# Performance work log

Hardware: AMD Instinct MI355X
Metric: run time of the kernel (lower is better)

## Reference

```python
import jax, jax.numpy as jnp
import numpy as np

N, D, K = 32768, 256, 4096
COMMITMENT_COST = 0.25
EPS_NORM = 1e-12  # matches torch F.normalize eps


def _l2_normalize(x):
    n = jnp.linalg.norm(x, axis=1, keepdims=True)
    return x / jnp.maximum(n, EPS_NORM)


def setup_inputs() -> dict:
    key = jax.random.key(0)
    k1, k2 = jax.random.split(key)
    inputs = jax.random.normal(k1, (N, D), dtype=jnp.float32)
    # xavier_uniform-like scale for the codebook
    bound = float(np.sqrt(6.0 / (K + D)))
    embeddings = jax.random.uniform(k2, (K, D), dtype=jnp.float32, minval=-bound, maxval=bound)
    return {"inputs": inputs, "embeddings": embeddings}


def reference(inputs, embeddings):
    flat = inputs.reshape(-1, D)
    x = _l2_normalize(flat)              # [N, D]
    e = _l2_normalize(embeddings)        # [K, D]
    # squared euclidean distance on normalized vectors
    distances = (jnp.sum(x * x, axis=1, keepdims=True)
                 + jnp.sum(e * e, axis=1)
                 - 2.0 * jnp.matmul(x, e.T))          # [N, K]
    encoding_indices = jnp.argmin(distances, axis=1)  # [N]
    quantized = embeddings[encoding_indices]          # gather, [N, D]
    # commitment loss (EMA variant: only commitment term is trained)
    e_latent_loss = jnp.mean((jax.lax.stop_gradient(quantized) - flat) ** 2)
    loss = COMMITMENT_COST * e_latent_loss
    # straight-through estimator
    quantized_st = flat + jax.lax.stop_gradient(quantized - flat)
    quantized_st = quantized_st.reshape(inputs.shape)
    return quantized_st, loss, encoding_indices
```

## Files before the change

### kernel.cpp

```cpp
#include <hip/hip_runtime.h>
#include <math.h>
#include <stdint.h>
#include <limits.h>

#define NPTS 32768
#define DIM  256
#define KCB  4096
#define NQ   (NPTS*DIM)

#define EPSN    1e-12f
#define MARGIN1 6.0e-4f
#define F16MIN  6.103515625e-05f
#define CAPB    4096
#define KINIT   0x7F800000FFFFFFFFull

typedef __attribute__((ext_vector_type(8))) _Float16 f16x8;
typedef __attribute__((ext_vector_type(4))) _Float16 f16x4;
typedef __attribute__((ext_vector_type(4))) float    f32x4;

#define WS_EH0   0u
#define WS_TRI   2097152u
#define WS_EMBT  0u
#define WS_SUME  4194304u
#define WS_EINV  4210688u
#define WS_XINV  4227072u
#define WS_IDX   4358144u
#define WS_RCA   4489216u
#define WS_RLA   4489232u
#define WS_RCB   4751376u
#define WS_RLB   4751392u
#define WS_BEST  4882464u
#define WS_LOSSP 4915232u

__device__ inline unsigned fbits(float f){ union{float f;unsigned u;}v; v.f=f; return v.u; }
__device__ inline float bitsf(unsigned u){ union{float f;unsigned u;}v; v.u=u; return v.f; }
__device__ inline uint64_t dbits(double d){ union{double d;uint64_t u;}v; v.d=d; return v.u; }
__device__ inline _Float16 g16(float v){
    return (fabsf(v) < F16MIN) ? (_Float16)0.0f : (_Float16)v;
}
__device__ inline void gload16(const void* src, void* lds){
    __builtin_amdgcn_global_load_lds((const __attribute__((address_space(1))) void*)src,
                                     (__attribute__((address_space(3))) void*)lds, 16, 0, 0);
}

__global__ void k_init(int* rca, int* rcb) {
    if (threadIdx.x == 0) { *rca = 0; *rcb = 0; }
}

__global__ __launch_bounds__(256) void k_norm_x(const float* __restrict__ x,
                                                float* __restrict__ xinv) {
    int w = threadIdx.x >> 6, l = threadIdx.x & 63;
    int row = blockIdx.x * 4 + w;
    float4 v = ((const float4*)x)[row * 64 + l];
    float s = v.x*v.x + v.y*v.y + v.z*v.z + v.w*v.w;
    #pragma unroll
    for (int o = 32; o; o >>= 1) s += __shfl_xor(s, o);
    if (l == 0) xinv[row] = 1.0f / fmaxf(sqrtf(s), EPSN);
}

__global__ __launch_bounds__(256) void k_norm_e(const float* __restrict__ e,
                                                _Float16* __restrict__ eh0,
                                                float* __restrict__ sume,
                                                float* __restrict__ einv) {
    int w = threadIdx.x >> 6, l = threadIdx.x & 63;
    int row = blockIdx.x * 4 + w;
    float4 v = ((const float4*)e)[row * 64 + l];
    float s = v.x*v.x + v.y*v.y + v.z*v.z + v.w*v.w;
    #pragma unroll
    for (int o = 32; o; o >>= 1) s += __shfl_xor(s, o);
    float inv = 1.0f / fmaxf(sqrtf(s), EPSN);
    float4 n = make_float4(v.x*inv, v.y*inv, v.z*inv, v.w*inv);
    f16x4 h0; h0[0]=g16(n.x); h0[1]=g16(n.y); h0[2]=g16(n.z); h0[3]=g16(n.w);
    ((f16x4*)eh0)[row * 64 + l] = h0;
    float s2 = n.x*n.x + n.y*n.y + n.z*n.z + n.w*n.w;
    #pragma unroll
    for (int o = 32; o; o >>= 1) s2 += __shfl_xor(s2, o);
    if (l == 0) { sume[row] = s2; einv[row] = inv; }
}

__global__ __launch_bounds__(256,2) void k_phase1(
    const float* __restrict__ x, const float* __restrict__ xinv,
    const _Float16* __restrict__ eh0,
    ulonglong2* __restrict__ tri)
{
    __shared__ __align__(16) _Float16 Bs[2][32 * DIM];
    const int tid = threadIdx.x;
    const int w = tid >> 6, l = tid & 63;
    const int l15 = l & 15, lhi = l >> 4;
    const int rowbase = (blockIdx.x >> 2) * 256 + w * 64;
    const int kbase   = (blockIdx.x & 3) * 1024;
    char* BsC = (char*)&Bs[0][0];

    f16x8 a[4][8];
    #pragma unroll
    for (int g = 0; g < 4; g++) {
        int row = rowbase + g*16 + l15;
        float xv = xinv[row];
        const float4* xr = (const float4*)(x + row * DIM);
        #pragma unroll
        for (int dc = 0; dc < 8; dc++) {
            float4 f0 = xr[dc*8 + lhi*2];
            float4 f1 = xr[dc*8 + lhi*2 + 1];
            f16x8 av;
            av[0]=g16(f0.x*xv); av[1]=g16(f0.y*xv);
            av[2]=g16(f0.z*xv); av[3]=g16(f0.w*xv);
            av[4]=g16(f1.x*xv); av[5]=g16(f1.y*xv);
            av[6]=g16(f1.z*xv); av[7]=g16(f1.w*xv);
            a[g][dc] = av;
        }
    }

    uint64_t t0[4], t1[4];
    float d2[4];
    #pragma unroll
    for (int g = 0; g < 4; g++) { t0[g]=KINIT; t1[g]=KINIT; d2[g]=INFINITY; }

    const char* sbase = (const char*)eh0 + (size_t)kbase * 512
                      + (size_t)(l & 31) * 512 + w*32 + (l >> 5)*16;
    auto stage = [&](int kt, int bufbyte) {
        const char* s = sbase + kt * 16384;
        #pragma unroll
        for (int p = 0; p < 4; p++) {
            gload16(s + p*128, BsC + bufbyte + ((p*256 + w*64) << 4));
        }
    };

    const int rb = lhi*512 + l15*16;
    const f32x4 zc = (f32x4){0.f, 0.f, 0.f, 0.f};

    auto compute = [&](int kt, int bufbyte) {
        f32x4 acc[4][2];
        #pragma unroll
        for (int dc = 0; dc < 8; dc++) {
            #pragma unroll
            for (int ni = 0; ni < 2; ni++) {
                f16x8 b = *(const f16x8*)(BsC + bufbyte + dc*2048 + ni*256 + rb);
                if (dc == 0) {
                    acc[0][ni] = __builtin_amdgcn_mfma_f32_16x16x32_f16(b, a[0][0], zc, 0, 0, 0);
                    acc[1][ni] = __builtin_amdgcn_mfma_f32_16x16x32_f16(b, a[1][0], zc, 0, 0, 0);
                    acc[2][ni] = __builtin_amdgcn_mfma_f32_16x16x32_f16(b, a[2][0], zc, 0, 0, 0);
                    acc[3][ni] = __builtin_amdgcn_mfma_f32_16x16x32_f16(b, a[3][0], zc, 0, 0, 0);
                } else {
                    acc[0][ni] = __builtin_amdgcn_mfma_f32_16x16x32_f16(b, a[0][dc], acc[0][ni], 0, 0, 0);
                    acc[1][ni] = __builtin_amdgcn_mfma_f32_16x16x32_f16(b, a[1][dc], acc[1][ni], 0, 0, 0);
                    acc[2][ni] = __builtin_amdgcn_mfma_f32_16x16x32_f16(b, a[2][dc], acc[2][ni], 0, 0, 0);
                    acc[3][ni] = __builtin_amdgcn_mfma_f32_16x16x32_f16(b, a[3][dc], acc[3][ni], 0, 0, 0);
                }
            }
        }

        #pragma unroll
        for (int ni = 0; ni < 2; ni++) {
            #pragma unroll
            for (int g = 0; g < 4; g++) {
                f32x4 v = acc[g][ni];
                float mx = fmaxf(fmaxf(v[0], v[1]), fmaxf(v[2], v[3]));
                if (5.0f - 2.0f*mx < d2[g]) {
                    #pragma unroll
                    for (int r = 0; r < 4; r++) {
                        float db = 5.0f - 2.0f*v[r];
                        if (db < d2[g]) {
                            int code = kbase + kt*32 + ni*16 + lhi*4 + r;
                            uint64_t key = ((uint64_t)fbits(db) << 32) | (unsigned)code;
                            if (key < t1[g]) {
                                d2[g] = bitsf((unsigned)(t1[g] >> 32));
                                if (key < t0[g]) { t1[g] = t0[g]; t0[g] = key; }
                                else t1[g] = key;
                            } else {
                                d2[g] = db;
                            }
                        }
                    }
                }
            }
        }
    };

    stage(0, 0);
    for (int kt = 0; kt < 32; kt += 2) {
        __syncthreads();
        stage(kt + 1, 16384);
        compute(kt, 0);
        __syncthreads();
        if (kt + 2 < 32) stage(kt + 2, 0);
        compute(kt + 1, 16384);
    }

    #pragma unroll
    for (int g = 0; g < 4; g++) {
        uint64_t a0 = t0[g], a1 = t1[g];
        float a2 = d2[g];
        #pragma unroll
        for (int m = 16; m < 64; m <<= 1) {
            uint64_t b0 = __shfl_xor(a0, m), b1 = __shfl_xor(a1, m);
            float    b2 = __shfl_xor(a2, m);
            uint64_t lo  = a0 < b0 ? a0 : b0;
            uint64_t hi0 = a0 < b0 ? b0 : a0;
            uint64_t lo1 = a1 < b1 ? a1 : b1;
            uint64_t mid = hi0 > lo1 ? hi0 : lo1;
            a1 = hi0 < lo1 ? hi0 : lo1;
            a0 = lo;
            a2 = fminf(fminf(a2, b2), bitsf((unsigned)(mid >> 32)));
        }
        t0[g] = a0; t1[g] = a1; d2[g] = a2;
    }

    if (lhi == 0) {
        const int split = blockIdx.x & 3;
        #pragma unroll
        for (int g = 0; g < 4; g++) {
            int row = rowbase + g*16 + l15;
            float d0 = bitsf((unsigned)(t0[g] >> 32));
            uint64_t flag = (d2[g] - d0 < MARGIN1) ? (1ull << 12) : 0ull;
            ulonglong2 ent;
            ent.x = t0[g];
            ent.y = t1[g] | flag;
            tri[(row << 2) | split] = ent;
        }
    }
}

__global__ __launch_bounds__(256) void k_merge(
    const ulonglong2* __restrict__ tri,
    int* __restrict__ idx,
    int* __restrict__ rca, int2* __restrict__ rla,
    int* __restrict__ rcb, int* __restrict__ rlb)
{
    int row = blockIdx.x * 256 + threadIdx.x;
    ulonglong2 e0 = tri[row*4 + 0];
    ulonglong2 e1 = tri[row*4 + 1];
    ulonglong2 e2 = tri[row*4 + 2];
    ulonglong2 e3 = tri[row*4 + 3];

    uint64_t c0 = e0.x, c1 = e0.y & ~0x1000ull;
    float c2 = INFINITY;
    auto fold = [&](uint64_t b0, uint64_t b1) {
        b1 &= ~0x1000ull;
        uint64_t lo  = c0 < b0 ? c0 : b0;
        uint64_t hi0 = c0 < b0 ? b0 : c0;
        uint64_t lo1 = c1 < b1 ? c1 : b1;
        uint64_t mid = hi0 > lo1 ? hi0 : lo1;
        c1 = hi0 < lo1 ? hi0 : lo1;
        c0 = lo;
        c2 = fminf(c2, bitsf((unsigned)(mid >> 32)));
    };
    fold(e1.x, e1.y);
    fold(e2.x, e2.y);
    fold(e3.x, e3.y);

    int k0 = (int)((unsigned)c0 & 0xFFFu);
    idx[row] = k0;
    float d0 = bitsf((unsigned)(c0 >> 32));
    float d1 = bitsf((unsigned)(c1 >> 32));
    bool lA = (d1 - d0 < MARGIN1);
    bool lB = (c2 - d0 < MARGIN1);
    if ((e0.y >> 12) & 1) lB |= (bitsf((unsigned)(e0.x >> 32)) - d0 < MARGIN1);
    if ((e1.y >> 12) & 1) lB |= (bitsf((unsigned)(e1.x >> 32)) - d0 < MARGIN1);
    if ((e2.y >> 12) & 1) lB |= (bitsf((unsigned)(e2.x >> 32)) - d0 < MARGIN1);
    if ((e3.y >> 12) & 1) lB |= (bitsf((unsigned)(e3.x >> 32)) - d0 < MARGIN1);

    if (lA) {
        int k1 = (int)((unsigned)c1 & 0xFFFu);
        int p = atomicAdd(rca, 1);
        if (p < NPTS) rla[p] = make_int2(row, k0 | (k1 << 12));
    }
    if (lB) {
        int q = atomicAdd(rcb, 1);
        if (q < CAPB) rlb[q] = row;
    }
}

__global__ __launch_bounds__(256) void k_transpose(const float* __restrict__ emb,
                                                   const float* __restrict__ einv,
                                                   float* __restrict__ embT) {
    __shared__ float tile[64][65];
    const int tid = threadIdx.x;
    const int kb = (blockIdx.x & 63) * 64;
    const int db = (blockIdx.x >> 6) * 64;
    #pragma unroll
    for (int s = 0; s < 16; s++) {
        int i = s * 256 + tid;
        int lk = i >> 6, ld = i & 63;
        tile[lk][ld] = emb[(kb + lk) * DIM + db + ld] * einv[kb + lk];
    }
    __syncthreads();
    #pragma unroll
    for (int s = 0; s < 16; s++) {
        int i = s * 256 + tid;
        int ld = i >> 6, lk = i & 63;
        embT[(db + ld) * KCB + kb + lk] = tile[lk][ld];
    }
}

__global__ __launch_bounds__(256) void k_cand(
    const float* __restrict__ x, const float* __restrict__ emb,
    const float* __restrict__ xinv, const float* __restrict__ einv,
    const float* __restrict__ sume,
    const int* __restrict__ rca, const int2* __restrict__ rla,
    int* __restrict__ idx)
{
    int cnt = *rca; if (cnt > NPTS) cnt = NPTS;
    const int w = threadIdx.x >> 6, l = threadIdx.x & 63;
    for (int r = blockIdx.x * 4 + w; r < cnt; r += gridDim.x * 4) {
        int2 ent = rla[r];
        int row = ent.x;
        int k0 = ent.y & 0xFFF, k1 = (ent.y >> 12) & 0xFFF;
        float xv = xinv[row];
        float4 xf = ((const float4*)x)[row * 64 + l];
        double x0 = (double)xf.x * (double)xv, x1 = (double)xf.y * (double)xv;
        double x2 = (double)xf.z * (double)xv, x3 = (double)xf.w * (double)xv;
        int ks[2] = {k0, k1};
        double d[2];
        #pragma unroll
        for (int c = 0; c < 2; c++) {
            int k = ks[c];
            float ev = einv[k];
            float4 e4 = ((const float4*)emb)[k * 64 + l];
            d[c] = x0 * (double)(e4.x * ev) + x1 * (double)(e4.y * ev)
                 + x2 * (double)(e4.z * ev) + x3 * (double)(e4.w * ev);
        }
        #pragma unroll
        for (int o = 32; o; o >>= 1) {
            d[0] += __shfl_xor(d[0], o);
            d[1] += __shfl_xor(d[1], o);
        }
        if (l == 0) {
            double dist0 = 4.0 + (double)sume[k0] - 2.0 * d[0];
            double dist1 = 4.0 + (double)sume[k1] - 2.0 * d[1];
            uint64_t key0 = (dbits(dist0) & 0xFFFFFFFFFFFFF000ull) | (unsigned)k0;
            uint64_t key1 = (dbits(dist1) & 0xFFFFFFFFFFFFF000ull) | (unsigned)k1;
            idx[row] = (int)((key0 < key1 ? key0 : key1) & 0xFFFull);
        }
    }
}

__global__ __launch_bounds__(256) void k_binit(uint64_t* __restrict__ bestu) {
    bestu[blockIdx.x * 256 + threadIdx.x] = ~0ull;
}

__global__ __launch_bounds__(256) void k_full(
    const float* __restrict__ x, const float* __restrict__ embT,
    const float* __restrict__ xinv, const float* __restrict__ sume,
    const int* __restrict__ rcb, const int* __restrict__ rlb,
    uint64_t* __restrict__ bestu)
{
    __shared__ float xs[DIM];
    int cnt = *rcb; if (cnt > CAPB) cnt = CAPB; if (cnt <= 0) return;
    int items = cnt * 16;
    const int tid = threadIdx.x;
    for (int item = blockIdx.x; item < items; item += gridDim.x) {
        int r = item >> 4, chunk = item & 15;
        int row = rlb[r];
        __syncthreads();
        xs[tid] = x[row * DIM + tid] * xinv[row];
        __syncthreads();
        int k = chunk * 256 + tid;
        const float* et = embT + k;
        double dp0 = 0, dp1 = 0, dp2 = 0, dp3 = 0;
        #pragma unroll 8
        for (int d = 0; d < DIM; d += 4) {
            dp0 += (double)xs[d+0] * (double)et[(d+0) * KCB];
            dp1 += (double)xs[d+1] * (double)et[(d+1) * KCB];
            dp2 += (double)xs[d+2] * (double)et[(d+2) * KCB];
            dp3 += (double)xs[d+3] * (double)et[(d+3) * KCB];
        }
        double dist = 4.0 + (double)sume[k] - 2.0 * ((dp0 + dp1) + (dp2 + dp3));
        uint64_t key = (dbits(dist) & 0xFFFFFFFFFFFFF000ull) | (unsigned)k;
        atomicMin((unsigned long long*)&bestu[r], (unsigned long long)key);
    }
}

__global__ __launch_bounds__(256) void k_ffin(const int* __restrict__ rcb,
                                              const int* __restrict__ rlb,
                                              const uint64_t* __restrict__ bestu,
                                              int* __restrict__ idx) {
    int cnt = *rcb; if (cnt > CAPB) cnt = CAPB;
    int i = blockIdx.x * 256 + threadIdx.x;
    if (i < cnt) idx[rlb[i]] = (int)(bestu[i] & 0xFFFull);
}

__global__ __launch_bounds__(256) void k_gather(const float* __restrict__ x,
                                                const float* __restrict__ emb,
                                                const int* __restrict__ idx,
                                                float* __restrict__ out,
                                                float* __restrict__ lossp) {
    int t = blockIdx.x * 256 + threadIdx.x;
    float ls = 0.f;
    #pragma unroll
    for (int s = 0; s < 4; ++s) {
        int i4 = t + s * 524288;
        int n = i4 >> 6, c4 = i4 & 63;
        int id = idx[n];
        float4 f = ((const float4*)x)[i4];
        float4 q = ((const float4*)emb)[id * 64 + c4];
        float dx = q.x - f.x, dy = q.y - f.y, dz = q.z - f.z, dw = q.w - f.w;
        float4 o = make_float4(f.x + dx, f.y + dy, f.z + dz, f.w + dw);
        ((float4*)out)[i4] = o;
        ls += dx*dx + dy*dy + dz*dz + dw*dw;
        if (c4 == 0) out[NQ + 1 + n] = (float)id;
    }
    #pragma unroll
    for (int o = 32; o; o >>= 1) ls += __shfl_xor(ls, o);
    __shared__ float wsum[4];
    int wid = threadIdx.x >> 6, lane = threadIdx.x & 63;
    if (lane == 0) wsum[wid] = ls;
    __syncthreads();
    if (threadIdx.x == 0) lossp[blockIdx.x] = wsum[0] + wsum[1] + wsum[2] + wsum[3];
}

__global__ __launch_bounds__(256) void k_finalize(const float* __restrict__ lossp,
                                                  float* __restrict__ out) {
    double s = 0;
    for (int i = threadIdx.x; i < 2048; i += 256) s += (double)lossp[i];
    #pragma unroll
    for (int o = 32; o; o >>= 1) s += __shfl_xor(s, o);
    __shared__ double wd[4];
    int wid = threadIdx.x >> 6, lane = threadIdx.x & 63;
    if (lane == 0) wd[wid] = s;
    __syncthreads();
    if (threadIdx.x == 0)
        out[NQ] = (float)(0.25 * ((wd[0] + wd[1] + wd[2] + wd[3]) / (double)NQ));
}

extern "C" void kernel_launch(void* const* d_in, const int* in_sizes, int n_in,
                              void* d_out, int out_size, void* d_ws, size_t ws_size,
                              hipStream_t stream) {
    const float* x   = (const float*)d_in[0];
    const float* emb = (const float*)d_in[1];
    char* ws = (char*)d_ws;
    _Float16* eh0 = (_Float16*)(ws + WS_EH0);
    ulonglong2* tri = (ulonglong2*)(ws + WS_TRI);
    float* embT  = (float*)(ws + WS_EMBT);
    float* sume  = (float*)(ws + WS_SUME);
    float* einv  = (float*)(ws + WS_EINV);
    float* xinv  = (float*)(ws + WS_XINV);
    int*   idx   = (int*)  (ws + WS_IDX);
    int*   rca   = (int*)  (ws + WS_RCA);
    int2*  rla   = (int2*) (ws + WS_RLA);
    int*   rcb   = (int*)  (ws + WS_RCB);
    int*   rlb   = (int*)  (ws + WS_RLB);
    uint64_t* bestu = (uint64_t*)(ws + WS_BEST);
    float* lossp = (float*)(ws + WS_LOSSP);
    float* out = (float*)d_out;

    hipLaunchKernelGGL(k_init,     dim3(1),          dim3(64),  0, stream, rca, rcb);
    hipLaunchKernelGGL(k_norm_x,   dim3(NPTS/4),     dim3(256), 0, stream, x, xinv);
    hipLaunchKernelGGL(k_norm_e,   dim3(KCB/4),      dim3(256), 0, stream, emb, eh0, sume, einv);
    hipLaunchKernelGGL(k_phase1,   dim3(NPTS/256*4), dim3(256), 0, stream,
                       x, xinv, eh0, tri);
    hipLaunchKernelGGL(k_merge,    dim3(NPTS/256),   dim3(256), 0, stream,
                       tri, idx, rca, rla, rcb, rlb);
    hipLaunchKernelGGL(k_transpose,dim3(256),        dim3(256), 0, stream, emb, einv, embT);
    hipLaunchKernelGGL(k_binit,    dim3(CAPB/256),   dim3(256), 0, stream, bestu);
    hipLaunchKernelGGL(k_cand,     dim3(1024),       dim3(256), 0, stream,
                       x, emb, xinv, einv, sume, rca, rla, idx);
    hipLaunchKernelGGL(k_full,     dim3(2048),       dim3(256), 0, stream,
                       x, embT, xinv, sume, rcb, rlb, bestu);
    hipLaunchKernelGGL(k_ffin,     dim3(16),         dim3(256), 0, stream, rcb, rlb, bestu, idx);
    hipLaunchKernelGGL(k_gather,   dim3(2048),       dim3(256), 0, stream,
                       x, emb, idx, out, lossp);
    hipLaunchKernelGGL(k_finalize, dim3(1),          dim3(256), 0, stream, lossp, out);
}
```

Before: 191.3 us.

## Drop codebook transpose, read row-major embeddings in full fallback, fold init kernels

Removes the k_transpose kernel that wrote a scaled, transposed codebook. k_full now reads the original row-major embeddings, with 8-lane groups each computing one codeword dot product and reducing via shuffles, then doing one atomicMin per group. The counter and bestu initialisation move into k_norm_e, removing two tiny launches. This trades the transpose pass and extra launches for per-element einv scaling in k_full and a different memory access pattern there.

```diff
diff --git a/kernel.cpp b/kernel.cpp
--- a/kernel.cpp
+++ b/kernel.cpp
@@ -20,7 +20,6 @@
 
 #define WS_EH0   0u
 #define WS_TRI   2097152u
-#define WS_EMBT  0u
 #define WS_SUME  4194304u
 #define WS_EINV  4210688u
 #define WS_XINV  4227072u
@@ -43,10 +42,6 @@
                                      (__attribute__((address_space(3))) void*)lds, 16, 0, 0);
 }
 
-__global__ void k_init(int* rca, int* rcb) {
-    if (threadIdx.x == 0) { *rca = 0; *rcb = 0; }
-}
-
 __global__ __launch_bounds__(256) void k_norm_x(const float* __restrict__ x,
                                                 float* __restrict__ xinv) {
     int w = threadIdx.x >> 6, l = threadIdx.x & 63;
@@ -61,7 +56,12 @@
 __global__ __launch_bounds__(256) void k_norm_e(const float* __restrict__ e,
                                                 _Float16* __restrict__ eh0,
                                                 float* __restrict__ sume,
-                                                float* __restrict__ einv) {
+                                                float* __restrict__ einv,
+                                                int* __restrict__ rca,
+                                                int* __restrict__ rcb,
+                                                uint64_t* __restrict__ bestu) {
+    if (blockIdx.x == 0 && threadIdx.x == 0) { *rca = 0; *rcb = 0; }
+    if (blockIdx.x < 16) bestu[blockIdx.x * 256 + threadIdx.x] = ~0ull;
     int w = threadIdx.x >> 6, l = threadIdx.x & 63;
     int row = blockIdx.x * 4 + w;
     float4 v = ((const float4*)e)[row * 64 + l];
@@ -270,28 +270,6 @@
     }
 }
 
-__global__ __launch_bounds__(256) void k_transpose(const float* __restrict__ emb,
-                                                   const float* __restrict__ einv,
-                                                   float* __restrict__ embT) {
-    __shared__ float tile[64][65];
-    const int tid = threadIdx.x;
-    const int kb = (blockIdx.x & 63) * 64;
-    const int db = (blockIdx.x >> 6) * 64;
-    #pragma unroll
-    for (int s = 0; s < 16; s++) {
-        int i = s * 256 + tid;
-        int lk = i >> 6, ld = i & 63;
-        tile[lk][ld] = emb[(kb + lk) * DIM + db + ld] * einv[kb + lk];
-    }
-    __syncthreads();
-    #pragma unroll
-    for (int s = 0; s < 16; s++) {
-        int i = s * 256 + tid;
-        int ld = i >> 6, lk = i & 63;
-        embT[(db + ld) * KCB + kb + lk] = tile[lk][ld];
-    }
-}
-
 __global__ __launch_bounds__(256) void k_cand(
     const float* __restrict__ x, const float* __restrict__ emb,
     const float* __restrict__ xinv, const float* __restrict__ einv,
@@ -334,39 +312,51 @@
     }
 }
 
-__global__ __launch_bounds__(256) void k_binit(uint64_t* __restrict__ bestu) {
-    bestu[blockIdx.x * 256 + threadIdx.x] = ~0ull;
-}
-
 __global__ __launch_bounds__(256) void k_full(
-    const float* __restrict__ x, const float* __restrict__ embT,
-    const float* __restrict__ xinv, const float* __restrict__ sume,
+    const float* __restrict__ x, const float* __restrict__ emb,
+    const float* __restrict__ xinv, const float* __restrict__ einv,
+    const float* __restrict__ sume,
     const int* __restrict__ rcb, const int* __restrict__ rlb,
     uint64_t* __restrict__ bestu)
 {
-    __shared__ float xs[DIM];
+    __shared__ __align__(16) float xs[DIM];
     int cnt = *rcb; if (cnt > CAPB) cnt = CAPB; if (cnt <= 0) return;
+    const int tid = threadIdx.x;
+    const int grp = tid >> 3, sub = tid & 7;
     int items = cnt * 16;
-    const int tid = threadIdx.x;
     for (int item = blockIdx.x; item < items; item += gridDim.x) {
         int r = item >> 4, chunk = item & 15;
         int row = rlb[r];
         __syncthreads();
         xs[tid] = x[row * DIM + tid] * xinv[row];
         __syncthreads();
-        int k = chunk * 256 + tid;
-        const float* et = embT + k;
-        double dp0 = 0, dp1 = 0, dp2 = 0, dp3 = 0;
-        #pragma unroll 8
-        for (int d = 0; d < DIM; d += 4) {
-            dp0 += (double)xs[d+0] * (double)et[(d+0) * KCB];
-            dp1 += (double)xs[d+1] * (double)et[(d+1) * KCB];
-            dp2 += (double)xs[d+2] * (double)et[(d+2) * KCB];
-            dp3 += (double)xs[d+3] * (double)et[(d+3) * KCB];
-        }
-        double dist = 4.0 + (double)sume[k] - 2.0 * ((dp0 + dp1) + (dp2 + dp3));
-        uint64_t key = (dbits(dist) & 0xFFFFFFFFFFFFF000ull) | (unsigned)k;
-        atomicMin((unsigned long long*)&bestu[r], (unsigned long long)key);
+        const float4* xs4 = (const float4*)xs;
+        uint64_t best = ~0ull;
+        #pragma unroll
+        for (int j = 0; j < 8; j++) {
+            int k = chunk * 256 + grp * 8 + j;
+            float ev = einv[k];
+            const float4* e4 = (const float4*)(emb + k * DIM);
+            double dp = 0;
+            #pragma unroll
+            for (int i = 0; i < 8; i++) {
+                float4 ef = e4[sub + i*8];
+                float4 xf = xs4[sub + i*8];
+                dp += (double)xf.x * (double)(ef.x * ev)
+                    + (double)xf.y * (double)(ef.y * ev)
+                    + (double)xf.z * (double)(ef.z * ev)
+                    + (double)xf.w * (double)(ef.w * ev);
+            }
+            #pragma unroll
+            for (int o = 4; o; o >>= 1) dp += __shfl_xor(dp, o);
+            if (sub == 0) {
+                double dist = 4.0 + (double)sume[k] - 2.0 * dp;
+                uint64_t key = (dbits(dist) & 0xFFFFFFFFFFFFF000ull) | (unsigned)k;
+                best = key < best ? key : best;
+            }
+        }
+        if (sub == 0)
+            atomicMin((unsigned long long*)&bestu[r], (unsigned long long)best);
     }
 }
 
@@ -430,7 +420,6 @@
     char* ws = (char*)d_ws;
     _Float16* eh0 = (_Float16*)(ws + WS_EH0);
     ulonglong2* tri = (ulonglong2*)(ws + WS_TRI);
-    float* embT  = (float*)(ws + WS_EMBT);
     float* sume  = (float*)(ws + WS_SUME);
     float* einv  = (float*)(ws + WS_EINV);
     float* xinv  = (float*)(ws + WS_XINV);
@@ -443,19 +432,17 @@
     float* lossp = (float*)(ws + WS_LOSSP);
     float* out = (float*)d_out;
 
-    hipLaunchKernelGGL(k_init,     dim3(1),          dim3(64),  0, stream, rca, rcb);
     hipLaunchKernelGGL(k_norm_x,   dim3(NPTS/4),     dim3(256), 0, stream, x, xinv);
-    hipLaunchKernelGGL(k_norm_e,   dim3(KCB/4),      dim3(256), 0, stream, emb, eh0, sume, einv);
+    hipLaunchKernelGGL(k_norm_e,   dim3(KCB/4),      dim3(256), 0, stream,
+                       emb, eh0, sume, einv, rca, rcb, bestu);
     hipLaunchKernelGGL(k_phase1,   dim3(NPTS/256*4), dim3(256), 0, stream,
                        x, xinv, eh0, tri);
     hipLaunchKernelGGL(k_merge,    dim3(NPTS/256),   dim3(256), 0, stream,
                        tri, idx, rca, rla, rcb, rlb);
-    hipLaunchKernelGGL(k_transpose,dim3(256),        dim3(256), 0, stream, emb, einv, embT);
-    hipLaunchKernelGGL(k_binit,    dim3(CAPB/256),   dim3(256), 0, stream, bestu);
     hipLaunchKernelGGL(k_cand,     dim3(1024),       dim3(256), 0, stream,
                        x, emb, xinv, einv, sume, rca, rla, idx);
     hipLaunchKernelGGL(k_full,     dim3(2048),       dim3(256), 0, stream,
-                       x, embT, xinv, sume, rcb, rlb, bestu);
+                       x, emb, xinv, einv, sume, rcb, rlb, bestu);
     hipLaunchKernelGGL(k_ffin,     dim3(16),         dim3(256), 0, stream, rcb, rlb, bestu, idx);
     hipLaunchKernelGGL(k_gather,   dim3(2048),       dim3(256), 0, stream,
                        x, emb, idx, out, lossp);
```

After: 177.8 us. 7.0% less time.
